# Kernel tuning notes

Measured on AMD Instinct MI355X. Metric: run time of the kernel, lower is better.

Reference implementation:

```python
import jax, jax.numpy as jnp
import numpy as np

N_NODES = 100000


def setup_inputs() -> dict:
    key = jax.random.key(0)
    k1, k2, k3, k4 = jax.random.split(key, 4)
    d = 64
    E = 1200000
    x = jax.random.normal(k1, (N_NODES, d), dtype=jnp.float32)
    edge_index = jax.random.randint(k2, (2, E), 0, N_NODES, dtype=jnp.int64)
    # GraphConv(dim, 1): lin_rel (with bias) applied to aggregated neighbors,
    # lin_root (no bias) applied to self features.
    W_rel = jax.random.normal(k3, (d, 1), dtype=jnp.float32) / np.sqrt(d)
    b_rel = jnp.zeros((1,), dtype=jnp.float32)
    W_root = jax.random.normal(k4, (d, 1), dtype=jnp.float32) / np.sqrt(d)
    return {"x": x, "edge_index": edge_index, "W_rel": W_rel, "b_rel": b_rel, "W_root": W_root}


def reference(x, edge_index, W_rel, b_rel, W_root):
    # x: [N, d], edge_index: [2, E] (row 0 = source j, row 1 = target i)
    src, dst = edge_index[0], edge_index[1]
    # sum-aggregate neighbor features: agg[i] = sum_{j: (j,i) in E} x[j]
    agg = jax.ops.segment_sum(x[src], dst, num_segments=N_NODES)  # [N, d]
    # GraphConv: lin_rel(agg) + lin_root(x) -> scalar score per node
    attn = agg @ W_rel + b_rel + x @ W_root  # [N, 1]
    return attn
```

## Files before the change

kernel.cpp:

```cpp
#include <hip/hip_runtime.h>

#define DIM 64
#define NPB 256
#define NPB_SHIFT 8
#define SEGCAP 4096
#define SEG_SHIFT 12
#define THREADS 512
#define K2_U 8
#define K2_EPB (THREADS * K2_U)
#define SRC_BITS 17
#define SRC_MASK ((1u << SRC_BITS) - 1u)
#define NODE_ROWS 128
#define OVF_CAP 8192

__global__ __launch_bounds__(THREADS)
void fused_kernel(const float4* __restrict__ x4,
                  const float4* __restrict__ Wrel4,
                  const float* __restrict__ b_rel,
                  const float4* __restrict__ Wroot4,
                  const int* __restrict__ ei,
                  float* __restrict__ s,
                  float* __restrict__ out,
                  int* __restrict__ cursor,
                  unsigned* __restrict__ bucket,
                  uint2* __restrict__ ovf,
                  int* __restrict__ ovf_cnt,
                  int E, int NB, int NBLK, int n) {
    __shared__ unsigned lpair[K2_EPB];
    __shared__ int  lga[K2_EPB];
    __shared__ int  hist[THREADS];
    __shared__ int  start[THREADS];
    __shared__ int  wsum[8];

    int tid = threadIdx.x;

    if (blockIdx.x < NBLK) {
        int blk = blockIdx.x;
        hist[tid] = 0;
        __syncthreads();

        int base = blk * K2_EPB + tid * K2_U;
        int dst[K2_U], src[K2_U], rnk[K2_U], bin[K2_U];
        int have = 0;

        if (base + K2_U <= E) {
            const int4* sv = (const int4*)ei;
            const int4* dv = (const int4*)(ei + E);
            int g = base >> 2;
            int4 s0 = sv[g], s1 = sv[g + 1];
            int4 d0 = dv[g], d1 = dv[g + 1];
            src[0] = s0.x; src[1] = s0.y; src[2] = s0.z; src[3] = s0.w;
            src[4] = s1.x; src[5] = s1.y; src[6] = s1.z; src[7] = s1.w;
            dst[0] = d0.x; dst[1] = d0.y; dst[2] = d0.z; dst[3] = d0.w;
            dst[4] = d1.x; dst[5] = d1.y; dst[6] = d1.z; dst[7] = d1.w;
            have = K2_U;
        } else {
            #pragma unroll
            for (int k = 0; k < K2_U; ++k) {
                int e = base + k;
                if (e < E) {
                    src[k] = ei[e];
                    dst[k] = ei[E + e];
                    have = k + 1;
                }
            }
        }

        #pragma unroll
        for (int k = 0; k < K2_U; ++k) {
            if (k < have) {
                bin[k] = dst[k] >> NPB_SHIFT;
                rnk[k] = atomicAdd(&hist[bin[k]], 1);
            }
        }
        __syncthreads();

        int h = hist[tid];
        if (tid < NB && h > 0) start[tid] = atomicAdd(&cursor[tid], h);

        int lane = tid & 63;
        int w = tid >> 6;
        int incl = h;
        #pragma unroll
        for (int off = 1; off < 64; off <<= 1) {
            int v = __shfl_up(incl, off);
            if (lane >= off) incl += v;
        }
        if (lane == 63) wsum[w] = incl;
        __syncthreads();

        int wb = 0;
        #pragma unroll
        for (int i = 0; i < 8; ++i) wb += (i < w) ? wsum[i] : 0;
        hist[tid] = wb + incl - h;
        __syncthreads();

        #pragma unroll
        for (int k = 0; k < K2_U; ++k) {
            if (k < have) {
                int b = bin[k];
                int slot = hist[b] + rnk[k];
                int gofs = start[b] + rnk[k];
                if (gofs < SEGCAP) {
                    lpair[slot] = ((unsigned)(dst[k] & (NPB - 1)) << SRC_BITS)
                                  | (unsigned)src[k];
                    lga[slot] = (b << SEG_SHIFT) + gofs;
                } else {
                    lga[slot] = -1;
                    int o = atomicAdd(ovf_cnt, 1);
                    if (o < OVF_CAP) ovf[o] = make_uint2((unsigned)dst[k],
                                                         (unsigned)src[k]);
                }
            }
        }
        __syncthreads();

        int nE = min(K2_EPB, E - blk * K2_EPB);
        for (int i = tid; i < nE; i += THREADS) {
            int ga = lga[i];
            if (ga >= 0) bucket[ga] = lpair[i];
        }
    } else {
        int nb = blockIdx.x - NBLK;
        int lane16 = tid & 15;
        int rg = tid >> 4;
        int rowbase = nb * NODE_ROWS + rg;
        float4 wr = Wrel4[lane16];
        float4 wt = Wroot4[lane16];
        float b0 = b_rel[0];

        float4 xv[4];
        int row[4];
        #pragma unroll
        for (int k = 0; k < 4; ++k) {
            row[k] = rowbase + k * 32;
            xv[k] = (row[k] < n) ? x4[(size_t)row[k] * (DIM / 4) + lane16]
                                 : make_float4(0.f, 0.f, 0.f, 0.f);
        }
        #pragma unroll
        for (int k = 0; k < 4; ++k) {
            float sr = xv[k].x * wr.x + xv[k].y * wr.y
                     + xv[k].z * wr.z + xv[k].w * wr.w;
            float st = xv[k].x * wt.x + xv[k].y * wt.y
                     + xv[k].z * wt.z + xv[k].w * wt.w;
            #pragma unroll
            for (int off = 1; off < 16; off <<= 1) {
                sr += __shfl_xor(sr, off);
                st += __shfl_xor(st, off);
            }
            if (lane16 == 0 && row[k] < n) {
                s[row[k]]   = sr;
                out[row[k]] = st + b0;
            }
        }
    }
}

__global__ __launch_bounds__(THREADS)
void gather_kernel(const int* __restrict__ cursor,
                   const unsigned* __restrict__ bucket,
                   const float* __restrict__ s,
                   float* __restrict__ out,
                   const uint2* __restrict__ ovf,
                   const int* __restrict__ ovf_cnt,
                   int n) {
    __shared__ float acc[NPB];
    int b = blockIdx.x;
    int tid = threadIdx.x;

    if (tid < NPB) acc[tid] = 0.f;
    __syncthreads();

    int total = min(cursor[b], SEGCAP);
    const unsigned* seg = bucket + ((size_t)b << SEG_SHIFT);
    const uint4* seg4 = (const uint4*)seg;

    int nvec = total >> 2;
    for (int i = tid; i < nvec; i += THREADS) {
        uint4 q = seg4[i];
        float v0 = s[q.x & SRC_MASK];
        float v1 = s[q.y & SRC_MASK];
        float v2 = s[q.z & SRC_MASK];
        float v3 = s[q.w & SRC_MASK];
        atomicAdd(&acc[q.x >> SRC_BITS], v0);
        atomicAdd(&acc[q.y >> SRC_BITS], v1);
        atomicAdd(&acc[q.z >> SRC_BITS], v2);
        atomicAdd(&acc[q.w >> SRC_BITS], v3);
    }
    for (int i = (nvec << 2) + tid; i < total; i += THREADS) {
        unsigned p = seg[i];
        atomicAdd(&acc[p >> SRC_BITS], s[p & SRC_MASK]);
    }

    int oc = min(*ovf_cnt, OVF_CAP);
    for (int j = tid; j < oc; j += THREADS) {
        uint2 p = ovf[j];
        if ((int)(p.x >> NPB_SHIFT) == b)
            atomicAdd(&acc[p.x & (NPB - 1)], s[p.y]);
    }
    __syncthreads();

    if (tid < NPB) {
        int g = b * NPB + tid;
        if (g < n) out[g] += acc[tid];
    }
}

extern "C" void kernel_launch(void* const* d_in, const int* in_sizes, int n_in,
                              void* d_out, int out_size, void* d_ws, size_t ws_size,
                              hipStream_t stream) {
    const float* x      = (const float*)d_in[0];
    const int*   ei     = (const int*)d_in[1];
    const float* W_rel  = (const float*)d_in[2];
    const float* b_rel  = (const float*)d_in[3];
    const float* W_root = (const float*)d_in[4];
    float* out = (float*)d_out;

    int n = out_size;
    int E = in_sizes[1] / 2;

    int NB = (n + NPB - 1) / NPB;

    float* s = (float*)d_ws;
    size_t off = ((size_t)n * 4 + 255) & ~(size_t)255;
    int* cursor = (int*)((char*)d_ws + off);
    int* ovf_cnt = cursor + NB;
    size_t zero_bytes = (size_t)(NB + 1) * sizeof(int);
    off += (zero_bytes + 255) & ~(size_t)255;
    uint2* ovf = (uint2*)((char*)d_ws + off);
    off += ((size_t)OVF_CAP * sizeof(uint2) + 255) & ~(size_t)255;
    unsigned* bucket = (unsigned*)((char*)d_ws + off);

    hipMemsetAsync(cursor, 0, zero_bytes, stream);

    int NBLK = (E + K2_EPB - 1) / K2_EPB;
    int NODEBLKS = (n + NODE_ROWS - 1) / NODE_ROWS;
    fused_kernel<<<NBLK + NODEBLKS, THREADS, 0, stream>>>(
        (const float4*)x, (const float4*)W_rel, b_rel, (const float4*)W_root,
        ei, s, out, cursor, bucket, ovf, ovf_cnt, E, NB, NBLK, n);

    gather_kernel<<<NB, THREADS, 0, stream>>>(cursor, bucket, s, out, ovf, ovf_cnt, n);
}
```

Measured before the change: 35.23 us.

## Replace global bucket cursors with per-strip local sorted segments and offset table

The scatter kernel no longer reserves space in global per-bucket segments through atomics. Each edge block instead writes its locally bucket-sorted edges contiguously as a strip, plus a per-bucket offset table. The gather kernel then walks every strip's sub-range for its bucket. This removes the memset, the global atomics, the scattered writes and the overflow path, but the gather does serial per-thread loops over short, scattered sub-ranges with fewer active threads.

```diff
diff --git a/kernel.cpp b/kernel.cpp
--- a/kernel.cpp
+++ b/kernel.cpp
@@ -3,15 +3,13 @@
 #define DIM 64
 #define NPB 256
 #define NPB_SHIFT 8
-#define SEGCAP 4096
-#define SEG_SHIFT 12
 #define THREADS 512
 #define K2_U 8
 #define K2_EPB (THREADS * K2_U)
+#define STRIP K2_EPB
 #define SRC_BITS 17
 #define SRC_MASK ((1u << SRC_BITS) - 1u)
 #define NODE_ROWS 128
-#define OVF_CAP 8192
 
 __global__ __launch_bounds__(THREADS)
 void fused_kernel(const float4* __restrict__ x4,
@@ -21,15 +19,11 @@
                   const int* __restrict__ ei,
                   float* __restrict__ s,
                   float* __restrict__ out,
-                  int* __restrict__ cursor,
                   unsigned* __restrict__ bucket,
-                  uint2* __restrict__ ovf,
-                  int* __restrict__ ovf_cnt,
+                  unsigned short* __restrict__ offs,
                   int E, int NB, int NBLK, int n) {
-    __shared__ unsigned lpair[K2_EPB];
-    __shared__ int  lga[K2_EPB];
+    __shared__ __align__(16) unsigned lpair[K2_EPB];
     __shared__ int  hist[THREADS];
-    __shared__ int  start[THREADS];
     __shared__ int  wsum[8];
 
     int tid = threadIdx.x;
@@ -76,7 +70,6 @@
         __syncthreads();
 
         int h = hist[tid];
-        if (tid < NB && h > 0) start[tid] = atomicAdd(&cursor[tid], h);
 
         int lane = tid & 63;
         int w = tid >> 6;
@@ -92,34 +85,29 @@
         int wb = 0;
         #pragma unroll
         for (int i = 0; i < 8; ++i) wb += (i < w) ? wsum[i] : 0;
-        hist[tid] = wb + incl - h;
+        int excl = wb + incl - h;
+
+        if (tid <= NB)
+            offs[(size_t)blk * (NB + 1) + tid] = (unsigned short)excl;
+
+        hist[tid] = excl;
         __syncthreads();
 
         #pragma unroll
         for (int k = 0; k < K2_U; ++k) {
             if (k < have) {
-                int b = bin[k];
-                int slot = hist[b] + rnk[k];
-                int gofs = start[b] + rnk[k];
-                if (gofs < SEGCAP) {
-                    lpair[slot] = ((unsigned)(dst[k] & (NPB - 1)) << SRC_BITS)
-                                  | (unsigned)src[k];
-                    lga[slot] = (b << SEG_SHIFT) + gofs;
-                } else {
-                    lga[slot] = -1;
-                    int o = atomicAdd(ovf_cnt, 1);
-                    if (o < OVF_CAP) ovf[o] = make_uint2((unsigned)dst[k],
-                                                         (unsigned)src[k]);
-                }
+                int slot = hist[bin[k]] + rnk[k];
+                lpair[slot] = ((unsigned)(dst[k] & (NPB - 1)) << SRC_BITS)
+                              | (unsigned)src[k];
             }
         }
         __syncthreads();
 
         int nE = min(K2_EPB, E - blk * K2_EPB);
-        for (int i = tid; i < nE; i += THREADS) {
-            int ga = lga[i];
-            if (ga >= 0) bucket[ga] = lpair[i];
-        }
+        int n4 = (nE + 3) >> 2;
+        const uint4* lp4 = (const uint4*)lpair;
+        uint4* dp4 = (uint4*)(bucket + (size_t)blk * STRIP);
+        for (int i = tid; i < n4; i += THREADS) dp4[i] = lp4[i];
     } else {
         int nb = blockIdx.x - NBLK;
         int lane16 = tid & 15;
@@ -157,13 +145,11 @@
 }
 
 __global__ __launch_bounds__(THREADS)
-void gather_kernel(const int* __restrict__ cursor,
+void gather_kernel(const unsigned short* __restrict__ offs,
                    const unsigned* __restrict__ bucket,
                    const float* __restrict__ s,
                    float* __restrict__ out,
-                   const uint2* __restrict__ ovf,
-                   const int* __restrict__ ovf_cnt,
-                   int n) {
+                   int NB, int NBLK, int n) {
     __shared__ float acc[NPB];
     int b = blockIdx.x;
     int tid = threadIdx.x;
@@ -171,32 +157,15 @@
     if (tid < NPB) acc[tid] = 0.f;
     __syncthreads();
 
-    int total = min(cursor[b], SEGCAP);
-    const unsigned* seg = bucket + ((size_t)b << SEG_SHIFT);
-    const uint4* seg4 = (const uint4*)seg;
-
-    int nvec = total >> 2;
-    for (int i = tid; i < nvec; i += THREADS) {
-        uint4 q = seg4[i];
-        float v0 = s[q.x & SRC_MASK];
-        float v1 = s[q.y & SRC_MASK];
-        float v2 = s[q.z & SRC_MASK];
-        float v3 = s[q.w & SRC_MASK];
-        atomicAdd(&acc[q.x >> SRC_BITS], v0);
-        atomicAdd(&acc[q.y >> SRC_BITS], v1);
-        atomicAdd(&acc[q.z >> SRC_BITS], v2);
-        atomicAdd(&acc[q.w >> SRC_BITS], v3);
-    }
-    for (int i = (nvec << 2) + tid; i < total; i += THREADS) {
-        unsigned p = seg[i];
-        atomicAdd(&acc[p >> SRC_BITS], s[p & SRC_MASK]);
-    }
-
-    int oc = min(*ovf_cnt, OVF_CAP);
-    for (int j = tid; j < oc; j += THREADS) {
-        uint2 p = ovf[j];
-        if ((int)(p.x >> NPB_SHIFT) == b)
-            atomicAdd(&acc[p.x & (NPB - 1)], s[p.y]);
+    for (int strip = tid; strip < NBLK; strip += THREADS) {
+        size_t ro = (size_t)strip * (NB + 1) + b;
+        int o0 = offs[ro];
+        int o1 = offs[ro + 1];
+        const unsigned* sp = bucket + (size_t)strip * STRIP;
+        for (int i = o0; i < o1; ++i) {
+            unsigned p = sp[i];
+            atomicAdd(&acc[p >> SRC_BITS], s[p & SRC_MASK]);
+        }
     }
     __syncthreads();
 
@@ -219,25 +188,19 @@
     int n = out_size;
     int E = in_sizes[1] / 2;
 
-    int NB = (n + NPB - 1) / NPB;
+    int NB   = (n + NPB - 1) / NPB;
+    int NBLK = (E + K2_EPB - 1) / K2_EPB;
 
     float* s = (float*)d_ws;
     size_t off = ((size_t)n * 4 + 255) & ~(size_t)255;
-    int* cursor = (int*)((char*)d_ws + off);
-    int* ovf_cnt = cursor + NB;
-    size_t zero_bytes = (size_t)(NB + 1) * sizeof(int);
-    off += (zero_bytes + 255) & ~(size_t)255;
-    uint2* ovf = (uint2*)((char*)d_ws + off);
-    off += ((size_t)OVF_CAP * sizeof(uint2) + 255) & ~(size_t)255;
+    unsigned short* offs = (unsigned short*)((char*)d_ws + off);
+    off += ((size_t)NBLK * (NB + 1) * 2 + 255) & ~(size_t)255;
     unsigned* bucket = (unsigned*)((char*)d_ws + off);
 
-    hipMemsetAsync(cursor, 0, zero_bytes, stream);
-
-    int NBLK = (E + K2_EPB - 1) / K2_EPB;
     int NODEBLKS = (n + NODE_ROWS - 1) / NODE_ROWS;
     fused_kernel<<<NBLK + NODEBLKS, THREADS, 0, stream>>>(
         (const float4*)x, (const float4*)W_rel, b_rel, (const float4*)W_root,
-        ei, s, out, cursor, bucket, ovf, ovf_cnt, E, NB, NBLK, n);
-
-    gather_kernel<<<NB, THREADS, 0, stream>>>(cursor, bucket, s, out, ovf, ovf_cnt, n);
+        ei, s, out, bucket, offs, E, NB, NBLK, n);
+
+    gather_kernel<<<NB, THREADS, 0, stream>>>(offs, bucket, s, out, NB, NBLK, n);
 }
```

After: 31.97 us. 1.1x faster.
